# Performance work log

Measured on AMD Instinct MI355X. Metric: run time of the kernel, lower is better.

## Reference

```python
import jax, jax.numpy as jnp
import numpy as np

HIDDEN = 1024
NUM_HEADS = 16
HEAD_DIM = HIDDEN // NUM_HEADS  # 64
B, S = 2, 2048


def setup_inputs() -> dict:
    key = jax.random.key(0)
    ks = jax.random.split(key, 10)
    sd = 1.0 / np.sqrt(HIDDEN)
    x = jax.random.normal(ks[0], (B, S, HIDDEN), dtype=jnp.float32)
    # per-head projections stacked over head axis: [H, hidden, head_dim]
    Wq = jax.random.normal(ks[1], (NUM_HEADS, HIDDEN, HEAD_DIM), dtype=jnp.float32) * sd
    Wk = jax.random.normal(ks[2], (NUM_HEADS, HIDDEN, HEAD_DIM), dtype=jnp.float32) * sd
    Wv = jax.random.normal(ks[3], (NUM_HEADS, HIDDEN, HEAD_DIM), dtype=jnp.float32) * sd
    bq = jax.random.normal(ks[4], (NUM_HEADS, HEAD_DIM), dtype=jnp.float32) * sd
    bk = jax.random.normal(ks[5], (NUM_HEADS, HEAD_DIM), dtype=jnp.float32) * sd
    bv = jax.random.normal(ks[6], (NUM_HEADS, HEAD_DIM), dtype=jnp.float32) * sd
    # output projection: [all_head_size, hidden]
    Wo = jax.random.normal(ks[7], (HIDDEN, HIDDEN), dtype=jnp.float32) * sd
    bo = jax.random.normal(ks[8], (HIDDEN,), dtype=jnp.float32) * sd
    return {"x": x, "Wq": Wq, "bq": bq, "Wk": Wk, "bk": bk,
            "Wv": Wv, "bv": bv, "Wo": Wo, "bo": bo}


def reference(x, Wq, bq, Wk, bk, Wv, bv, Wo, bo):
    # Fused-across-heads equivalent of the per-head Python loop.
    # q,k,v: [B, H, S, Dh]
    q = jnp.einsum('bsd,hde->bhse', x, Wq) + bq[None, :, None, :]
    k = jnp.einsum('bsd,hde->bhse', x, Wk) + bk[None, :, None, :]
    v = jnp.einsum('bsd,hde->bhse', x, Wv) + bv[None, :, None, :]
    scale = 1.0 / jnp.sqrt(jnp.asarray(HEAD_DIM, dtype=x.dtype))
    scores = jnp.einsum('bhse,bhte->bhst', q, k) * scale  # [B,H,S,S]
    probs = jax.nn.softmax(scores, axis=-1)               # dropout=0 (eval)
    ctx = jnp.einsum('bhst,bhte->bhse', probs, v)         # [B,H,S,Dh]
    # concat heads on last dim (head order matches torch.cat over heads)
    ctx = jnp.transpose(ctx, (0, 2, 1, 3)).reshape(x.shape[0], x.shape[1], -1)
    out = ctx @ Wo + bo                                   # output projection
    return out
```

## Files before the change

### kernel.cpp

```cpp
#include <hip/hip_runtime.h>
#include <cstdint>

typedef unsigned short u16;
typedef __attribute__((ext_vector_type(8))) short short8;
typedef __attribute__((ext_vector_type(4))) short short4v;
typedef __attribute__((ext_vector_type(4))) float f32x4;
typedef __attribute__((ext_vector_type(4))) unsigned short u16x4;

__device__ __forceinline__ u16 f2bf(float x) {
    unsigned int u = __float_as_uint(x);
    u += 0x7fffu + ((u >> 16) & 1u);
    return (u16)(u >> 16);
}

__device__ __forceinline__ float fexp2(float x) {
#if __has_builtin(__builtin_amdgcn_exp2f)
    return __builtin_amdgcn_exp2f(x);
#else
    return exp2f(x);
#endif
}

__device__ __forceinline__ unsigned pack_bf16(float a, float b) {
    unsigned ua = __float_as_uint(a) + 0x8000u;
    unsigned ub = __float_as_uint(b) + 0x8000u;
    return __builtin_amdgcn_perm(ub, ua, 0x07060302u);
}

#if __has_builtin(__builtin_amdgcn_mfma_f32_16x16x16bf16_1k)
__device__ __forceinline__ f32x4 mfma16(short4v a, short4v b, f32x4 c) {
    return __builtin_amdgcn_mfma_f32_16x16x16bf16_1k(a, b, c, 0, 0, 0);
}
#else
__device__ __forceinline__ f32x4 mfma16(short4v a, short4v b, f32x4 c) {
    short8 a8 = {a[0], a[1], a[2], a[3], 0, 0, 0, 0};
    short8 b8 = {b[0], b[1], b[2], b[3], 0, 0, 0, 0};
    return __builtin_amdgcn_mfma_f32_16x16x32_bf16(a8, b8, c, 0, 0, 0);
}
#endif

__device__ __forceinline__ void gload_lds16(const u16* g, u16* l) {
    __builtin_amdgcn_global_load_lds(
        (const __attribute__((address_space(1))) void*)(g),
        (__attribute__((address_space(3))) void*)(l),
        16, 0, 0);
}

__global__ __launch_bounds__(256) void prep_kernel(
    const float* __restrict__ x,
    const float* __restrict__ Wq, const float* __restrict__ Wk,
    const float* __restrict__ Wv, const float* __restrict__ Wo,
    u16* __restrict__ xb, u16* __restrict__ wqkv, u16* __restrict__ wot)
{
    __shared__ u16 tile[64][65];
    const int z = blockIdx.z;
    const int tc = threadIdx.x & 63, tr = threadIdx.x >> 6;

    if (z == 1) {
        const int blk = blockIdx.y * 16 + blockIdx.x;
        const int base = (blk * 256 + threadIdx.x) * 4;
        #pragma unroll
        for (int i = 0; i < 16; ++i) {
            const int idx = base + i * 262144;
            float4 v = *(const float4*)(x + idx);
            u16x4 o;
            o.x = f2bf(v.x); o.y = f2bf(v.y); o.z = f2bf(v.z); o.w = f2bf(v.w);
            *(u16x4*)(xb + idx) = o;
        }
        return;
    }

    const float* src;
    u16* dst;
    int C, R, rb, cb;
    if (z == 0) {
        src = Wo; dst = wot; C = 1024; R = 1024;
        rb = blockIdx.x * 64; cb = blockIdx.y * 64;
    } else {
        const float* W = (z == 2) ? Wq : (z == 3) ? Wk : Wv;
        const int head = blockIdx.y;
        src = W + head * 65536;
        dst = wqkv + (size_t)(z - 2) * 1048576 + head * 65536;
        C = 64; R = 1024;
        rb = blockIdx.x * 64; cb = 0;
    }
    #pragma unroll
    for (int i = 0; i < 64; i += 4)
        tile[tr + i][tc] = f2bf(src[(size_t)(rb + tr + i) * C + (cb + tc)]);
    __syncthreads();
    #pragma unroll
    for (int i = 0; i < 64; i += 4)
        dst[(size_t)(cb + tr + i) * R + (rb + tc)] = tile[tc][tr + i];
}

__global__ __launch_bounds__(256, 3) void gemm_qkv_kernel(
    const u16* __restrict__ X, const u16* __restrict__ W,
    const float* __restrict__ bq, const float* __restrict__ bk,
    const float* __restrict__ bv,
    u16* __restrict__ qo, u16* __restrict__ ko, u16* __restrict__ vto)
{
    __shared__ __align__(16) u16 As[128 * 32];
    __shared__ __align__(16) u16 Bs[128 * 32];
    const int tid = threadIdx.x;
    const int lane = tid & 63;
    const int wv = tid >> 6;
    const int wm = wv & 1, wn = wv >> 1;
    const int m0 = blockIdx.y * 128;
    const int n0 = blockIdx.x * 128;
    const int c = lane & 15, qd = lane >> 4;

    f32x4 acc[4][4];
    #pragma unroll
    for (int a = 0; a < 4; ++a)
        #pragma unroll
        for (int b2 = 0; b2 < 4; ++b2) acc[a][b2] = f32x4{0.f, 0.f, 0.f, 0.f};

    const u16* Xb = X + (size_t)m0 * 1024;
    const u16* Wb = W + (size_t)n0 * 1024;

    for (int kt = 0; kt < 1024; kt += 32) {
        #pragma unroll
        for (int i = 0; i < 2; ++i) {
            int slot = i * 256 + tid;
            int row = slot >> 2, part = slot & 3;
            gload_lds16(Xb + (size_t)row * 1024 + kt + part * 8, &As[slot * 8]);
            gload_lds16(Wb + (size_t)row * 1024 + kt + part * 8, &Bs[slot * 8]);
        }
        __syncthreads();
        short8 af[4], bf[4];
        #pragma unroll
        for (int mt = 0; mt < 4; ++mt)
            af[mt] = *(const short8*)&As[(wm * 64 + mt * 16 + c) * 32 + qd * 8];
        #pragma unroll
        for (int nt = 0; nt < 4; ++nt)
            bf[nt] = *(const short8*)&Bs[(wn * 64 + nt * 16 + c) * 32 + qd * 8];
        #pragma unroll
        for (int mt = 0; mt < 4; ++mt)
            #pragma unroll
            for (int nt = 0; nt < 4; ++nt)
                acc[mt][nt] = __builtin_amdgcn_mfma_f32_16x16x32_bf16(af[mt], bf[nt], acc[mt][nt], 0, 0, 0);
        __syncthreads();
    }

    #pragma unroll
    for (int mt = 0; mt < 4; ++mt) {
        const int mbase = m0 + wm * 64 + mt * 16 + qd * 4;
        const int b = mbase >> 11;
        #pragma unroll
        for (int nt = 0; nt < 4; ++nt) {
            const int n = n0 + wn * 64 + nt * 16 + c;
            const int mat = n >> 10;
            const int idx = n & 1023;
            const int h = idx >> 6, e = idx & 63;
            const float bias = (mat == 0 ? bq : (mat == 1 ? bk : bv))[idx];
            if (mat == 2) {
                const int s = mbase & 2047;
                u16x4 pv;
                pv.x = f2bf(acc[mt][nt][0] + bias);
                pv.y = f2bf(acc[mt][nt][1] + bias);
                pv.z = f2bf(acc[mt][nt][2] + bias);
                pv.w = f2bf(acc[mt][nt][3] + bias);
                *(u16x4*)(vto + ((((size_t)(b * 16 + h) * 128 + (s >> 4)) * 64 + e) * 16
                                 + (s & 15))) = pv;
            } else {
                const float scale = (mat == 0) ? 0.18033688011112042f : 1.0f;
                u16* dst = (mat == 0) ? qo : ko;
                #pragma unroll
                for (int r = 0; r < 4; ++r) {
                    const int s = (mbase + r) & 2047;
                    dst[((size_t)((b * 16 + h) * 2048 + s)) * 64 + e] =
                        f2bf((acc[mt][nt][r] + bias) * scale);
                }
            }
        }
    }
}

__global__ __launch_bounds__(256, 3) void flash_kernel(
    const u16* __restrict__ Q,
    const u16* __restrict__ K,
    const u16* __restrict__ V2,
    u16* __restrict__ ctx)
{
    __shared__ __align__(16) char pool[49152];
    u16* stage = (u16*)pool;
    float (*Os)[64][66] = (float (*)[64][66])pool;
    float (*Ls)[64] = (float (*)[64])(pool + 33792);

    const int tid = threadIdx.x, lane = tid & 63, w = tid >> 6;
    const int c = lane & 15, qd = lane >> 4;
    const int bid = blockIdx.x;
    const int r5 = bid & 31;
    const int bh = (r5 & 7) * 4 + (r5 >> 3);
    const int q0 = (bid >> 5) * 64;
    const int b = bh >> 4, h = bh & 15;
    const u16* Qh = Q + (size_t)bh * 2048 * 64;
    const u16* Kh = K + (size_t)bh * 2048 * 64;
    const u16* Vh = V2 + (size_t)bh * 128 * 1024;

    u16* Kst = stage + w * 6144;
    u16* Vst = Kst + 3072;

    const int krow8 = lane >> 3;
    const int kgc = (lane & 7) ^ (krow8 & 7);

    short8 qf[4][2];
    #pragma unroll
    for (int qb = 0; qb < 4; ++qb)
        #pragma unroll
        for (int kb = 0; kb < 2; ++kb)
            qf[qb][kb] = *(const short8*)&Qh[(size_t)(q0 + qb * 16 + c) * 64 + kb * 32 + qd * 8];

    f32x4 o[4][4];
    f32x4 ol[4];
    #pragma unroll
    for (int mt = 0; mt < 4; ++mt)
        #pragma unroll
        for (int qb = 0; qb < 4; ++qb) o[mt][qb] = f32x4{0.f, 0.f, 0.f, 0.f};
    #pragma unroll
    for (int qb = 0; qb < 4; ++qb) ol[qb] = f32x4{0.f, 0.f, 0.f, 0.f};
    const short4v ones = {(short)0x3F80, (short)0x3F80, (short)0x3F80, (short)0x3F80};

    #pragma unroll
    for (int pit = 0; pit < 2; ++pit) {
        const int t0 = w * 512 + pit * 16;
        #pragma unroll
        for (int j = 0; j < 2; ++j) {
            const int row = j * 8 + krow8;
            gload_lds16(Kh + (size_t)(t0 + row) * 64 + kgc * 8,
                        Kst + pit * 1024 + j * 512 + lane * 8);
            gload_lds16(Vh + (size_t)(t0 >> 4) * 1024 + (j * 64 + lane) * 8,
                        Vst + pit * 1024 + j * 512 + lane * 8);
        }
    }

    int cur = 0;
    for (int it = 0; it < 32; ++it) {
        u16* Kb = Kst + cur * 1024;
        u16* Vb = Vst + cur * 1024;

        __builtin_amdgcn_s_waitcnt(0xF74);
        __builtin_amdgcn_sched_barrier(0);

        short8 kf[2];
        #pragma unroll
        for (int kb = 0; kb < 2; ++kb)
            kf[kb] = *(const short8*)&Kb[c * 64 + ((4 * kb + qd) ^ (c & 7)) * 8];
        short4v vf[4];
        #pragma unroll
        for (int mt = 0; mt < 4; ++mt)
            vf[mt] = *(const short4v*)&Vb[(mt * 16 + c) * 16 + qd * 4];

        __builtin_amdgcn_sched_barrier(0);

        {
            const int itn = (it + 2) & 31;
            const int t0n = w * 512 + itn * 16;
            const int nslot = (cur >= 1) ? cur - 1 : 2;
            u16* Kn = Kst + nslot * 1024;
            u16* Vn = Vst + nslot * 1024;
            #pragma unroll
            for (int j = 0; j < 2; ++j) {
                const int row = j * 8 + krow8;
                gload_lds16(Kh + (size_t)(t0n + row) * 64 + kgc * 8,
                            Kn + j * 512 + lane * 8);
                gload_lds16(Vh + (size_t)(t0n >> 4) * 1024 + (j * 64 + lane) * 8,
                            Vn + j * 512 + lane * 8);
            }
        }

        f32x4 sc[4];
        #pragma unroll
        for (int qb = 0; qb < 4; ++qb) {
            sc[qb] = f32x4{0.f, 0.f, 0.f, 0.f};
            sc[qb] = __builtin_amdgcn_mfma_f32_16x16x32_bf16(kf[0], qf[qb][0], sc[qb], 0, 0, 0);
            sc[qb] = __builtin_amdgcn_mfma_f32_16x16x32_bf16(kf[1], qf[qb][1], sc[qb], 0, 0, 0);
        }

        short4v pb[4];
        #pragma unroll
        for (int qb = 0; qb < 4; ++qb) {
            float p0 = fexp2(sc[qb][0]);
            float p1 = fexp2(sc[qb][1]);
            float p2 = fexp2(sc[qb][2]);
            float p3 = fexp2(sc[qb][3]);
            unsigned d0 = pack_bf16(p0, p1);
            unsigned d1 = pack_bf16(p2, p3);
            union { unsigned u[2]; short4v s; } pu;
            pu.u[0] = d0; pu.u[1] = d1;
            pb[qb] = pu.s;
        }

        #pragma unroll
        for (int qb = 0; qb < 4; ++qb) {
            #pragma unroll
            for (int mt = 0; mt < 4; ++mt)
                o[mt][qb] = mfma16(vf[mt], pb[qb], o[mt][qb]);
            ol[qb] = mfma16(ones, pb[qb], ol[qb]);
        }

        cur = (cur == 2) ? 0 : cur + 1;
    }

    __builtin_amdgcn_s_waitcnt(0xF70);
    __syncthreads();
    if (qd == 0) {
        #pragma unroll
        for (int qb = 0; qb < 4; ++qb) Ls[w][qb * 16 + c] = ol[qb][0];
    }

    if (w >= 2) {
        float (*S)[66] = Os[w - 2];
        #pragma unroll
        for (int mt = 0; mt < 4; ++mt)
            #pragma unroll
            for (int qb = 0; qb < 4; ++qb)
                #pragma unroll
                for (int r = 0; r < 4; ++r)
                    S[mt * 16 + qd * 4 + r][qb * 16 + c] = o[mt][qb][r];
    }
    __syncthreads();
    if (w < 2) {
        float (*S)[66] = Os[w];
        #pragma unroll
        for (int mt = 0; mt < 4; ++mt)
            #pragma unroll
            for (int qb = 0; qb < 4; ++qb)
                #pragma unroll
                for (int r = 0; r < 4; ++r)
                    o[mt][qb][r] += S[mt * 16 + qd * 4 + r][qb * 16 + c];
    }
    __syncthreads();
    if (w == 1) {
        float (*S)[66] = Os[0];
        #pragma unroll
        for (int mt = 0; mt < 4; ++mt)
            #pragma unroll
            for (int qb = 0; qb < 4; ++qb)
                #pragma unroll
                for (int r = 0; r < 4; ++r)
                    S[mt * 16 + qd * 4 + r][qb * 16 + c] = o[mt][qb][r];
    }
    __syncthreads();
    if (w == 0) {
        float (*S)[66] = Os[0];
        float inv[4];
        #pragma unroll
        for (int qb = 0; qb < 4; ++qb) {
            int q = qb * 16 + c;
            float l = (Ls[0][q] + Ls[1][q]) + (Ls[2][q] + Ls[3][q]);
            inv[qb] = __builtin_amdgcn_rcpf(l);
        }
        #pragma unroll
        for (int mt = 0; mt < 4; ++mt)
            #pragma unroll
            for (int qb = 0; qb < 4; ++qb) {
                u16x4 ov;
                #pragma unroll
                for (int r = 0; r < 4; ++r) {
                    float v = (o[mt][qb][r] + S[mt * 16 + qd * 4 + r][qb * 16 + c]) * inv[qb];
                    ((u16*)&ov)[r] = f2bf(v);
                }
                *(u16x4*)&ctx[((size_t)(b * 2048 + q0 + qb * 16 + c)) * 1024
                              + h * 64 + mt * 16 + qd * 4] = ov;
            }
    }
}

__global__ __launch_bounds__(256, 4) void gemm_out_kernel(
    const u16* __restrict__ A, const u16* __restrict__ Wt,
    const float* __restrict__ bo, float* __restrict__ out)
{
    __shared__ __align__(16) u16 As[64 * 32];
    __shared__ __align__(16) u16 Bs[128 * 32];
    const int tid = threadIdx.x;
    const int lane = tid & 63;
    const int wv = tid >> 6;
    const int wm = wv & 1, wn = wv >> 1;
    const int m0 = blockIdx.x * 64;
    const int n0 = blockIdx.y * 128;
    const int c = lane & 15, qd = lane >> 4;

    f32x4 acc[2][4];
    #pragma unroll
    for (int a = 0; a < 2; ++a)
        #pragma unroll
        for (int b2 = 0; b2 < 4; ++b2) acc[a][b2] = f32x4{0.f, 0.f, 0.f, 0.f};

    const u16* Ab = A + (size_t)m0 * 1024;
    const u16* Wb = Wt + (size_t)n0 * 1024;

    for (int kt = 0; kt < 1024; kt += 32) {
        {
            int row = tid >> 2, part = tid & 3;
            gload_lds16(Ab + (size_t)row * 1024 + kt + part * 8, &As[tid * 8]);
        }
        #pragma unroll
        for (int i = 0; i < 2; ++i) {
            int slot = i * 256 + tid;
            int row = slot >> 2, part = slot & 3;
            gload_lds16(Wb + (size_t)row * 1024 + kt + part * 8, &Bs[slot * 8]);
        }
        __syncthreads();
        short8 af[2], bf[4];
        #pragma unroll
        for (int mt = 0; mt < 2; ++mt)
            af[mt] = *(const short8*)&As[(wm * 32 + mt * 16 + c) * 32 + qd * 8];
        #pragma unroll
        for (int nt = 0; nt < 4; ++nt)
            bf[nt] = *(const short8*)&Bs[(wn * 64 + nt * 16 + c) * 32 + qd * 8];
        #pragma unroll
        for (int mt = 0; mt < 2; ++mt)
            #pragma unroll
            for (int nt = 0; nt < 4; ++nt)
                acc[mt][nt] = __builtin_amdgcn_mfma_f32_16x16x32_bf16(af[mt], bf[nt], acc[mt][nt], 0, 0, 0);
        __syncthreads();
    }

    #pragma unroll
    for (int mt = 0; mt < 2; ++mt) {
        const int mbase = m0 + wm * 32 + mt * 16 + qd * 4;
        #pragma unroll
        for (int nt = 0; nt < 4; ++nt) {
            const int n = n0 + wn * 64 + nt * 16 + c;
            const float bias = bo[n];
            #pragma unroll
            for (int r = 0; r < 4; ++r)
                out[(size_t)(mbase + r) * 1024 + n] = acc[mt][nt][r] + bias;
        }
    }
}

extern "C" void kernel_launch(void* const* d_in, const int* in_sizes, int n_in,
                              void* d_out, int out_size, void* d_ws, size_t ws_size,
                              hipStream_t stream) {
    const float* x  = (const float*)d_in[0];
    const float* Wq = (const float*)d_in[1];
    const float* bq = (const float*)d_in[2];
    const float* Wk = (const float*)d_in[3];
    const float* bk = (const float*)d_in[4];
    const float* Wv = (const float*)d_in[5];
    const float* bv = (const float*)d_in[6];
    const float* Wo = (const float*)d_in[7];
    const float* bo = (const float*)d_in[8];
    float* out = (float*)d_out;

    u16* ws    = (u16*)d_ws;
    u16* xb    = ws;
    u16* wqkv  = xb + 4096 * 1024;
    u16* wot   = wqkv + 3072 * 1024;
    u16* qws   = wot + 1024 * 1024;
    u16* kws   = qws + 4194304;
    u16* v2ws  = kws + 4194304;
    u16* ctxws = v2ws + 4194304;

    prep_kernel<<<dim3(16, 16, 5), 256, 0, stream>>>(x, Wq, Wk, Wv, Wo, xb, wqkv, wot);
    gemm_qkv_kernel<<<dim3(24, 32), 256, 0, stream>>>(xb, wqkv, bq, bk, bv, qws, kws, v2ws);
    flash_kernel<<<1024, 256, 0, stream>>>(qws, kws, v2ws, ctxws);
    gemm_out_kernel<<<dim3(64, 8), 256, 0, stream>>>(ctxws, wot, bo, out);
}
```

Baseline: 192.7 us.

## Load V fragments directly to registers and compute row sums with VALU

V tiles are now read from global memory straight into registers and double-buffered across loop iterations, so they are no longer staged through LDS. The LDS pool shrinks to hold only K staging, which may allow more resident blocks. The softmax denominator is now accumulated as scalar sums of the probabilities plus cross-lane shuffles, replacing the extra ones-vector MFMA. The catch is that direct register loads of V sit in the critical path without the async LDS copy, and vmcnt waits now cover both streams.

After: 190.7 us. Within noise of the previous version (-1.0%).

```diff
diff --git a/kernel.cpp b/kernel.cpp
--- a/kernel.cpp
+++ b/kernel.cpp
@@ -182,7 +182,7 @@
     const u16* __restrict__ V2,
     u16* __restrict__ ctx)
 {
-    __shared__ __align__(16) char pool[49152];
+    __shared__ __align__(16) char pool[34816];
     u16* stage = (u16*)pool;
     float (*Os)[64][66] = (float (*)[64][66])pool;
     float (*Ls)[64] = (float (*)[64])(pool + 33792);
@@ -198,11 +198,11 @@
     const u16* Kh = K + (size_t)bh * 2048 * 64;
     const u16* Vh = V2 + (size_t)bh * 128 * 1024;
 
-    u16* Kst = stage + w * 6144;
-    u16* Vst = Kst + 3072;
+    u16* Kst = stage + w * 3072;
 
     const int krow8 = lane >> 3;
     const int kgc = (lane & 7) ^ (krow8 & 7);
+    const int voff = c * 16 + qd * 4;
 
     short8 qf[4][2];
     #pragma unroll
@@ -212,32 +212,37 @@
             qf[qb][kb] = *(const short8*)&Qh[(size_t)(q0 + qb * 16 + c) * 64 + kb * 32 + qd * 8];
 
     f32x4 o[4][4];
-    f32x4 ol[4];
+    float lsum[4];
     #pragma unroll
     for (int mt = 0; mt < 4; ++mt)
         #pragma unroll
         for (int qb = 0; qb < 4; ++qb) o[mt][qb] = f32x4{0.f, 0.f, 0.f, 0.f};
     #pragma unroll
-    for (int qb = 0; qb < 4; ++qb) ol[qb] = f32x4{0.f, 0.f, 0.f, 0.f};
-    const short4v ones = {(short)0x3F80, (short)0x3F80, (short)0x3F80, (short)0x3F80};
-
-    #pragma unroll
-    for (int pit = 0; pit < 2; ++pit) {
-        const int t0 = w * 512 + pit * 16;
-        #pragma unroll
-        for (int j = 0; j < 2; ++j) {
-            const int row = j * 8 + krow8;
-            gload_lds16(Kh + (size_t)(t0 + row) * 64 + kgc * 8,
-                        Kst + pit * 1024 + j * 512 + lane * 8);
-            gload_lds16(Vh + (size_t)(t0 >> 4) * 1024 + (j * 64 + lane) * 8,
-                        Vst + pit * 1024 + j * 512 + lane * 8);
-        }
+    for (int qb = 0; qb < 4; ++qb) lsum[qb] = 0.f;
+
+    #pragma unroll
+    for (int j = 0; j < 2; ++j) {
+        const int row = j * 8 + krow8;
+        gload_lds16(Kh + (size_t)(w * 512 + row) * 64 + kgc * 8,
+                    Kst + j * 512 + lane * 8);
+    }
+    short4v vA[4], vB[4];
+    {
+        const u16* vb = Vh + (size_t)(w * 32) * 1024 + voff;
+        #pragma unroll
+        for (int mt = 0; mt < 4; ++mt)
+            vA[mt] = *(const short4v*)(vb + mt * 256);
+    }
+    #pragma unroll
+    for (int j = 0; j < 2; ++j) {
+        const int row = j * 8 + krow8;
+        gload_lds16(Kh + (size_t)(w * 512 + 16 + row) * 64 + kgc * 8,
+                    Kst + 1024 + j * 512 + lane * 8);
     }
 
     int cur = 0;
-    for (int it = 0; it < 32; ++it) {
+    auto body = [&](int it, short4v (&VC)[4], short4v (&VN)[4]) {
         u16* Kb = Kst + cur * 1024;
-        u16* Vb = Vst + cur * 1024;
 
         __builtin_amdgcn_s_waitcnt(0xF74);
         __builtin_amdgcn_sched_barrier(0);
@@ -246,26 +251,26 @@
         #pragma unroll
         for (int kb = 0; kb < 2; ++kb)
             kf[kb] = *(const short8*)&Kb[c * 64 + ((4 * kb + qd) ^ (c & 7)) * 8];
-        short4v vf[4];
-        #pragma unroll
-        for (int mt = 0; mt < 4; ++mt)
-            vf[mt] = *(const short4v*)&Vb[(mt * 16 + c) * 16 + qd * 4];
 
         __builtin_amdgcn_sched_barrier(0);
 
+        {
+            const int itn = (it + 1) & 31;
+            const u16* vb = Vh + (size_t)(w * 32 + itn) * 1024 + voff;
+            #pragma unroll
+            for (int mt = 0; mt < 4; ++mt)
+                VN[mt] = *(const short4v*)(vb + mt * 256);
+        }
         {
             const int itn = (it + 2) & 31;
             const int t0n = w * 512 + itn * 16;
             const int nslot = (cur >= 1) ? cur - 1 : 2;
             u16* Kn = Kst + nslot * 1024;
-            u16* Vn = Vst + nslot * 1024;
             #pragma unroll
             for (int j = 0; j < 2; ++j) {
                 const int row = j * 8 + krow8;
                 gload_lds16(Kh + (size_t)(t0n + row) * 64 + kgc * 8,
                             Kn + j * 512 + lane * 8);
-                gload_lds16(Vh + (size_t)(t0n >> 4) * 1024 + (j * 64 + lane) * 8,
-                            Vn + j * 512 + lane * 8);
             }
         }
 
@@ -284,6 +289,7 @@
             float p1 = fexp2(sc[qb][1]);
             float p2 = fexp2(sc[qb][2]);
             float p3 = fexp2(sc[qb][3]);
+            lsum[qb] += (p0 + p1) + (p2 + p3);
             unsigned d0 = pack_bf16(p0, p1);
             unsigned d1 = pack_bf16(p2, p3);
             union { unsigned u[2]; short4v s; } pu;
@@ -292,21 +298,30 @@
         }
 
         #pragma unroll
-        for (int qb = 0; qb < 4; ++qb) {
+        for (int qb = 0; qb < 4; ++qb)
             #pragma unroll
             for (int mt = 0; mt < 4; ++mt)
-                o[mt][qb] = mfma16(vf[mt], pb[qb], o[mt][qb]);
-            ol[qb] = mfma16(ones, pb[qb], ol[qb]);
-        }
+                o[mt][qb] = mfma16(VC[mt], pb[qb], o[mt][qb]);
 
         cur = (cur == 2) ? 0 : cur + 1;
+    };
+
+    for (int it2 = 0; it2 < 16; ++it2) {
+        body(2 * it2, vA, vB);
+        body(2 * it2 + 1, vB, vA);
     }
 
     __builtin_amdgcn_s_waitcnt(0xF70);
     __syncthreads();
+
+    #pragma unroll
+    for (int qb = 0; qb < 4; ++qb) {
+        lsum[qb] += __shfl_xor(lsum[qb], 16, 64);
+        lsum[qb] += __shfl_xor(lsum[qb], 32, 64);
+    }
     if (qd == 0) {
         #pragma unroll
-        for (int qb = 0; qb < 4; ++qb) Ls[w][qb * 16 + c] = ol[qb][0];
+        for (int qb = 0; qb < 4; ++qb) Ls[w][qb * 16 + c] = lsum[qb];
     }
 
     if (w >= 2) {
```
